# Performance work log

Measured on AMD Instinct MI355X. Metric: run time of the kernel, lower is better.

## Reference

```python
import jax, jax.numpy as jnp
import numpy as np

TOKEN_DIM = 512
ATTN_DIM = 512
NUM_HEADS = 8
MLP_SIZE = 2048
EPS = 1e-6


def setup_inputs() -> dict:
    key = jax.random.key(0)
    ks = jax.random.split(key, 9)
    s_tok = 1.0 / np.sqrt(TOKEN_DIM)
    s_att = 1.0 / np.sqrt(ATTN_DIM)
    s_mlp = 1.0 / np.sqrt(MLP_SIZE)
    return {
        "inputs": jax.random.normal(ks[0], (2, 4096, TOKEN_DIM), dtype=jnp.float32),
        "Wq": jax.random.uniform(ks[1], (TOKEN_DIM, ATTN_DIM), jnp.float32, -s_tok, s_tok),
        "Wk": jax.random.uniform(ks[2], (TOKEN_DIM, ATTN_DIM), jnp.float32, -s_tok, s_tok),
        "Wv": jax.random.uniform(ks[3], (TOKEN_DIM, ATTN_DIM), jnp.float32, -s_tok, s_tok),
        "Wo": jax.random.uniform(ks[4], (ATTN_DIM, TOKEN_DIM), jnp.float32, -s_att, s_att),
        "W1": jax.random.uniform(ks[5], (TOKEN_DIM, MLP_SIZE), jnp.float32, -s_tok, s_tok),
        "b1": jax.random.uniform(ks[6], (MLP_SIZE,), jnp.float32, -s_tok, s_tok),
        "W2": jax.random.uniform(ks[7], (MLP_SIZE, TOKEN_DIM), jnp.float32, -s_mlp, s_mlp),
        "b2": jax.random.uniform(ks[8], (TOKEN_DIM,), jnp.float32, -s_mlp, s_mlp),
        "ln_att_g": jnp.ones((TOKEN_DIM,), jnp.float32),
        "ln_att_b": jnp.zeros((TOKEN_DIM,), jnp.float32),
        "ln_mlp_g": jnp.ones((TOKEN_DIM,), jnp.float32),
        "ln_mlp_b": jnp.zeros((TOKEN_DIM,), jnp.float32),
    }


def _layernorm(x, g, b):
    mu = jnp.mean(x, axis=-1, keepdims=True)
    var = jnp.mean(jnp.square(x - mu), axis=-1, keepdims=True)
    return (x - mu) * jax.lax.rsqrt(var + EPS) * g + b


def _attention(x, Wq, Wk, Wv, Wo):
    B, N, _ = x.shape
    H, Dh = NUM_HEADS, ATTN_DIM // NUM_HEADS
    # project then split heads: (B, N, H, Dh) -> (B, H, N, Dh)
    q = (x @ Wq).reshape(B, N, H, Dh).transpose(0, 2, 1, 3)
    k = (x @ Wk).reshape(B, N, H, Dh).transpose(0, 2, 1, 3)
    v = (x @ Wv).reshape(B, N, H, Dh).transpose(0, 2, 1, 3)
    scale = Dh ** -0.5
    scores = jnp.einsum("bhnd,bhmd->bhnm", q, k) * scale  # full NxN scores
    attn = jax.nn.softmax(scores, axis=-1)
    out = jnp.einsum("bhnm,bhmd->bhnd", attn, v)
    out = out.transpose(0, 2, 1, 3).reshape(B, N, ATTN_DIM)
    return out @ Wo


def reference(inputs, Wq, Wk, Wv, Wo, W1, b1, W2, b2,
              ln_att_g, ln_att_b, ln_mlp_g, ln_mlp_b):
    x = _layernorm(inputs, ln_att_g, ln_att_b)
    x = _attention(x, Wq, Wk, Wv, Wo)
    y = x + inputs
    z = _layernorm(y, ln_mlp_g, ln_mlp_b)
    z = jax.nn.gelu(z @ W1 + b1, approximate=False) @ W2 + b2
    return z + y
```

## Files before the change

kernel.cpp:

```cpp
#include <hip/hip_runtime.h>
#include <hip/hip_bf16.h>
#include <cmath>


typedef unsigned short u16;
typedef float  f32x4  __attribute__((ext_vector_type(4)));
typedef short  bf16x8 __attribute__((ext_vector_type(8)));
typedef u16    u16x4  __attribute__((ext_vector_type(4)));

#define DEV __device__ __forceinline__
#define AS1(p) ((const __attribute__((address_space(1))) void*)(p))
#define AS3(p) ((__attribute__((address_space(3))) void*)(p))

static constexpr int Mrows = 8192;
static constexpr int Dtok  = 512;
static constexpr int Fmlp  = 2048;
static constexpr float LOG2E = 1.44269504088896340736f;

DEV u16 f2b(float f) {
  union { float f; unsigned u; } v; v.f = f;
  unsigned r = v.u + 0x7fffu + ((v.u >> 16) & 1u);
  return (u16)(r >> 16);
}

DEV unsigned cvtpk(float a, float b) {
  unsigned r;
  asm("v_cvt_pk_bf16_f32 %0, %1, %2" : "=v"(r) : "v"(a), "v"(b));
  return r;
}

DEV void plswap16(unsigned &a, unsigned &b) {
  asm("v_permlane16_swap_b32 %0, %1" : "+v"(a), "+v"(b));
}

DEV float ex2(float x) {
#if __has_builtin(__builtin_amdgcn_exp2f)
  return __builtin_amdgcn_exp2f(x);
#else
  float r; asm("v_exp_f32 %0, %1" : "=v"(r) : "v"(x)); return r;
#endif
}

DEV f32x4 mfma32(bf16x8 a, bf16x8 b, f32x4 c) {
  return __builtin_amdgcn_mfma_f32_16x16x32_bf16(a, b, c, 0, 0, 0);
}

__global__ __launch_bounds__(256) void convert_all(
    const float* __restrict__ Wq, const float* __restrict__ Wk,
    const float* __restrict__ Wv, const float* __restrict__ Wo,
    const float* __restrict__ W1, const float* __restrict__ W2,
    u16* __restrict__ Wqt, u16* __restrict__ Wkt, u16* __restrict__ Wvt,
    u16* __restrict__ Wot, u16* __restrict__ W1t, u16* __restrict__ W2t,
    float qscale) {
  int bid = blockIdx.x;
  const float* src; u16* dst; int K, N; float sc = 1.0f;
  if (bid < 1024)      { src = Wq; dst = Wqt; K = 512;  N = 512;  sc = qscale; }
  else if (bid < 2048) { src = Wk; dst = Wkt; K = 512;  N = 512;  bid -= 1024; }
  else if (bid < 3072) { src = Wv; dst = Wvt; K = 512;  N = 512;  bid -= 2048; }
  else if (bid < 4096) { src = Wo; dst = Wot; K = 512;  N = 512;  bid -= 3072; }
  else if (bid < 8192) { src = W1; dst = W1t; K = 512;  N = 2048; bid -= 4096; }
  else                 { src = W2; dst = W2t; K = 2048; N = 512;  bid -= 8192; }
  const int idx = bid * 256 + threadIdx.x;
  const int k = idx / N, n = idx - k * N;
  dst[(size_t)n * K + k] = f2b(src[idx] * sc);
}

__global__ __launch_bounds__(256) void ln_kernel(const float* __restrict__ x,
                                                 const float* __restrict__ g,
                                                 const float* __restrict__ b,
                                                 u16* __restrict__ o) {
  const int row = blockIdx.x, tid = threadIdx.x;
  float2 v = ((const float2*)(x + (size_t)row * 512))[tid];
  float s = v.x + v.y, ss = v.x * v.x + v.y * v.y;
#pragma unroll
  for (int off = 32; off > 0; off >>= 1) {
    s  += __shfl_down(s, off);
    ss += __shfl_down(ss, off);
  }
  __shared__ float ps[4], pss[4];
  const int wave = tid >> 6, lane = tid & 63;
  if (lane == 0) { ps[wave] = s; pss[wave] = ss; }
  __syncthreads();
  const float S  = ps[0] + ps[1] + ps[2] + ps[3];
  const float SS = pss[0] + pss[1] + pss[2] + pss[3];
  const float mean = S * (1.0f / 512.0f);
  const float var  = SS * (1.0f / 512.0f) - mean * mean;
  const float rstd = rsqrtf(var + 1e-6f);
  const float2 gg = ((const float2*)g)[tid];
  const float2 bb = ((const float2*)b)[tid];
  ushort2 ov;
  ov.x = f2b((v.x - mean) * rstd * gg.x + bb.x);
  ov.y = f2b((v.y - mean) * rstd * gg.y + bb.y);
  ((ushort2*)(o + (size_t)row * 512))[tid] = ov;
}

template <int EPI, int BM>
__global__ __launch_bounds__(256) void gemm_kernel(
    const u16* __restrict__ A, const u16* __restrict__ Bt,
    u16* __restrict__ outb, u16* __restrict__ outbK, u16* __restrict__ outbV,
    float* __restrict__ outf,
    const float* __restrict__ bias, const float* __restrict__ resid,
    int M, int N, int K) {
  __shared__ u16 Al[BM * 32];
  __shared__ u16 Bl[128 * 32];
  constexpr int WM = BM / 2;
  const int tid = threadIdx.x;
  const int wave = tid >> 6, lane = tid & 63;
  const int lhi = lane >> 4, llo = lane & 15;
  const int wr = wave >> 1, wc = wave & 1;
  const int m0 = blockIdx.y * BM, n0 = blockIdx.x * 128;

  f32x4 acc[BM / 32][4] = {};

  for (int k0 = 0; k0 < K; k0 += 32) {
#pragma unroll
    for (int i = 0; i < BM / 64; ++i) {
      const int rb = i * 64 + wave * 16;
      const u16* sa = A + (size_t)(m0 + rb + (lane >> 2)) * K + k0 + (lane & 3) * 8;
      __builtin_amdgcn_global_load_lds(AS1(sa), AS3(&Al[rb * 32]), 16, 0, 0);
    }
#pragma unroll
    for (int i = 0; i < 2; ++i) {
      const int rb = i * 64 + wave * 16;
      const u16* sb = Bt + (size_t)(n0 + rb + (lane >> 2)) * K + k0 + (lane & 3) * 8;
      __builtin_amdgcn_global_load_lds(AS1(sb), AS3(&Bl[rb * 32]), 16, 0, 0);
    }
    __syncthreads();
    bf16x8 af[BM / 32], bfr[4];
#pragma unroll
    for (int mi = 0; mi < BM / 32; ++mi)
      af[mi] = *(const bf16x8*)&Al[(wr * WM + mi * 16 + llo) * 32 + lhi * 8];
#pragma unroll
    for (int ni = 0; ni < 4; ++ni)
      bfr[ni] = *(const bf16x8*)&Bl[(wc * 64 + ni * 16 + llo) * 32 + lhi * 8];
#pragma unroll
    for (int mi = 0; mi < BM / 32; ++mi)
#pragma unroll
      for (int ni = 0; ni < 4; ++ni)
        acc[mi][ni] = __builtin_amdgcn_mfma_f32_16x16x32_bf16(af[mi], bfr[ni],
                                                              acc[mi][ni], 0, 0, 0);
    __syncthreads();
  }

  if constexpr (EPI == 5) {
    if (n0 < 1024) {
      u16* dst = (n0 < 512) ? outb : outbK;
      const int c0 = (n0 & 511) + wc * 64;
#pragma unroll
      for (int mi = 0; mi < BM / 32; ++mi)
#pragma unroll
        for (int r = 0; r < 4; ++r) {
          const size_t grow = (size_t)m0 + wr * WM + mi * 16 + lhi * 4 + r;
#pragma unroll
          for (int ni = 0; ni < 4; ++ni)
            dst[grow * 512 + c0 + ni * 16 + llo] = f2b(acc[mi][ni][r]);
        }
    } else {
      const int bb = m0 >> 12;
      const int nb = (m0 & 4095) + wr * WM + lhi * 4;
#pragma unroll
      for (int mi = 0; mi < BM / 32; ++mi)
#pragma unroll
        for (int ni = 0; ni < 4; ++ni) {
          const int gcol = (n0 - 1024) + wc * 64 + ni * 16 + llo;
          u16x4 pk;
#pragma unroll
          for (int r = 0; r < 4; ++r) pk[r] = f2b(acc[mi][ni][r]);
          u16* dst = outbV + (((size_t)(bb * 8 + (gcol >> 6))) * 64 + (gcol & 63)) * 4096
                           + nb + mi * 16;
          *(u16x4*)dst = pk;
        }
    }
  } else {
#pragma unroll
    for (int mi = 0; mi < BM / 32; ++mi) {
#pragma unroll
      for (int r = 0; r < 4; ++r) {
        const size_t grow = (size_t)m0 + wr * WM + mi * 16 + lhi * 4 + r;
#pragma unroll
        for (int ni = 0; ni < 4; ++ni) {
          const int gcol = n0 + wc * 64 + ni * 16 + llo;
          float v = acc[mi][ni][r];
          if (EPI == 0) {
            outb[grow * N + gcol] = f2b(v);
          } else if (EPI == 1) {
            v += bias[gcol];
            v = 0.5f * v * (1.0f + erff(v * 0.70710678118654752f));
            outb[grow * N + gcol] = f2b(v);
          } else if (EPI == 2) {
            v += resid[grow * N + gcol];
            outf[grow * N + gcol] = v;
          } else {
            v += bias[gcol] + resid[grow * N + gcol];
            outf[grow * N + gcol] = v;
          }
        }
      }
    }
  }
}

__global__ __launch_bounds__(256) void attn_kernel(const u16* __restrict__ Q,
                                                   const u16* __restrict__ Kg,
                                                   const u16* __restrict__ VT,
                                                   u16* __restrict__ O) {
  const int qt = blockIdx.x, bh = blockIdx.y;
  const int b = bh >> 3, h = bh & 7;
  const int tid = threadIdx.x, wave = tid >> 6, lane = tid & 63;
  const int lhi = lane >> 4, llo = lane & 15;

  __shared__ u16 Kl[2][4096];
  __shared__ u16 Vl[2][4096];

  const size_t rowbase = (size_t)b * 4096;
  const int col0 = h * 64;
  const int q0 = qt * 128;

  bf16x8 qf0[2], qf1[2];
  {
    const u16* qp0 = Q + (rowbase + q0 + wave * 32 + llo) * 512 + col0 + lhi * 8;
    qf0[0] = *(const bf16x8*)qp0;
    qf0[1] = *(const bf16x8*)(qp0 + 32);
    const u16* qp1 = qp0 + (size_t)16 * 512;
    qf1[0] = *(const bf16x8*)qp1;
    qf1[1] = *(const bf16x8*)(qp1 + 32);
  }

  const int srow8 = lane >> 3;
  const int kcsw  = ((lane & 7) ^ srow8) * 8;
  const u16* kbase0 = Kg + (rowbase + wave * 16 + srow8) * 512 + col0 + kcsw;
  const u16* kbase1 = kbase0 + (size_t)8 * 512;
  const u16* vbase0 = VT + ((size_t)bh * 64 + wave * 16 + srow8) * 4096 + kcsw;
  const u16* vbase1 = vbase0 + (size_t)8 * 4096;

  const int xr = (llo & 7) << 4;
  const int ka0 = (16 * lhi) ^ xr;
  const int ka1 = (16 * (4 + lhi)) ^ xr;
  const int csig = ((lhi & 1) << 1) | (lhi >> 1);
  const int vb0 = 16 * (csig ^ (llo & 7));
  const int vb1 = 16 * ((csig | 4) ^ (llo & 7));

  const bf16x8 ones = {(short)0x3F80, (short)0x3F80, (short)0x3F80, (short)0x3F80,
                       (short)0x3F80, (short)0x3F80, (short)0x3F80, (short)0x3F80};

  f32x4 o0[4] = {}, o1[4] = {};
  f32x4 o40 = {}, o41 = {};

  auto stage = [&](int kvr, int B) {
    __builtin_amdgcn_global_load_lds(AS1(kbase0 + (size_t)kvr * 512),
                                     AS3(&Kl[B][wave * 1024]), 16, 0, 0);
    __builtin_amdgcn_global_load_lds(AS1(kbase1 + (size_t)kvr * 512),
                                     AS3(&Kl[B][wave * 1024 + 512]), 16, 0, 0);
    __builtin_amdgcn_global_load_lds(AS1(vbase0 + kvr),
                                     AS3(&Vl[B][wave * 1024]), 16, 0, 0);
    __builtin_amdgcn_global_load_lds(AS1(vbase1 + kvr),
                                     AS3(&Vl[B][wave * 1024 + 512]), 16, 0, 0);
  };

  auto packP = [&](const f32x4* stj, bf16x8& Bv0, bf16x8& Bv1) {
    unsigned a0 = cvtpk(ex2(stj[0][0]), ex2(stj[0][1]));
    unsigned a1 = cvtpk(ex2(stj[0][2]), ex2(stj[0][3]));
    unsigned b0 = cvtpk(ex2(stj[1][0]), ex2(stj[1][1]));
    unsigned b1 = cvtpk(ex2(stj[1][2]), ex2(stj[1][3]));
    unsigned c0 = cvtpk(ex2(stj[2][0]), ex2(stj[2][1]));
    unsigned c1 = cvtpk(ex2(stj[2][2]), ex2(stj[2][3]));
    unsigned d0 = cvtpk(ex2(stj[3][0]), ex2(stj[3][1]));
    unsigned d1 = cvtpk(ex2(stj[3][2]), ex2(stj[3][3]));
    plswap16(a0, b0); plswap16(a1, b1);
    plswap16(c0, d0); plswap16(c1, d1);
    union UB { unsigned u[4]; bf16x8 v; } X, Y;
    X.u[0] = a0; X.u[1] = a1; X.u[2] = b0; X.u[3] = b1;
    Y.u[0] = c0; Y.u[1] = c1; Y.u[2] = d0; Y.u[3] = d1;
    Bv0 = X.v; Bv1 = Y.v;
  };

  auto compute = [&](int B) {
    const char* klb = (const char*)&Kl[B][0] + llo * 128;
    const char* vlb = (const char*)&Vl[B][0] + llo * 128;
    f32x4 st0[4], st1[4];
    __builtin_amdgcn_s_setprio(1);
#pragma unroll
    for (int jt = 0; jt < 4; ++jt) {
      bf16x8 kf0 = *(const bf16x8*)(klb + jt * 2048 + ka0);
      bf16x8 kf1 = *(const bf16x8*)(klb + jt * 2048 + ka1);
      f32x4 z0 = {}, z1 = {};
      z0 = mfma32(kf0, qf0[0], z0); z0 = mfma32(kf1, qf0[1], z0);
      z1 = mfma32(kf0, qf1[0], z1); z1 = mfma32(kf1, qf1[1], z1);
      st0[jt] = z0; st1[jt] = z1;
    }
    __builtin_amdgcn_s_setprio(0);
    bf16x8 P00, P01, P10, P11;
    packP(st0, P00, P01);
    packP(st1, P10, P11);
    __builtin_amdgcn_s_setprio(1);
    o40 = mfma32(ones, P00, o40); o40 = mfma32(ones, P01, o40);
    o41 = mfma32(ones, P10, o41); o41 = mfma32(ones, P11, o41);
#pragma unroll
    for (int dt = 0; dt < 4; ++dt) {
      bf16x8 vf0 = *(const bf16x8*)(vlb + dt * 2048 + vb0);
      bf16x8 vf1 = *(const bf16x8*)(vlb + dt * 2048 + vb1);
      o0[dt] = mfma32(vf0, P00, o0[dt]); o0[dt] = mfma32(vf1, P01, o0[dt]);
      o1[dt] = mfma32(vf0, P10, o1[dt]); o1[dt] = mfma32(vf1, P11, o1[dt]);
    }
    __builtin_amdgcn_s_setprio(0);
  };

  stage(0, 0);
  __syncthreads();
  for (int kv0 = 0; kv0 < 4096; kv0 += 128) {
    stage(kv0 + 64, 1);
    compute(0);
    __syncthreads();
    if (kv0 + 128 < 4096) stage(kv0 + 128, 0);
    compute(1);
    __syncthreads();
  }

  {
    const float inv = 1.0f / o40[0];
    u16* op = O + (rowbase + q0 + wave * 32 + llo) * 512 + col0 + 4 * lhi;
#pragma unroll
    for (int dt = 0; dt < 4; ++dt) {
      u16x4 pk;
#pragma unroll
      for (int r = 0; r < 4; ++r) pk[r] = f2b(o0[dt][r] * inv);
      *(u16x4*)(op + dt * 16) = pk;
    }
  }
  {
    const float inv = 1.0f / o41[0];
    u16* op = O + (rowbase + q0 + wave * 32 + 16 + llo) * 512 + col0 + 4 * lhi;
#pragma unroll
    for (int dt = 0; dt < 4; ++dt) {
      u16x4 pk;
#pragma unroll
      for (int r = 0; r < 4; ++r) pk[r] = f2b(o1[dt][r] * inv);
      *(u16x4*)(op + dt * 16) = pk;
    }
  }
}

extern "C" void kernel_launch(void* const* d_in, const int* in_sizes, int n_in,
                              void* d_out, int out_size, void* d_ws, size_t ws_size,
                              hipStream_t stream) {
  const float* inputs = (const float*)d_in[0];
  const float* Wq  = (const float*)d_in[1];
  const float* Wk  = (const float*)d_in[2];
  const float* Wv  = (const float*)d_in[3];
  const float* Wo  = (const float*)d_in[4];
  const float* W1  = (const float*)d_in[5];
  const float* b1  = (const float*)d_in[6];
  const float* W2  = (const float*)d_in[7];
  const float* b2  = (const float*)d_in[8];
  const float* g1  = (const float*)d_in[9];
  const float* be1 = (const float*)d_in[10];
  const float* g2  = (const float*)d_in[11];
  const float* be2 = (const float*)d_in[12];
  float* out = (float*)d_out;

  const int M = Mrows, D = Dtok, F = Fmlp;

  char* w = (char*)d_ws;
  u16* xln  = (u16*)w;  w += (size_t)M * D * 2;
  u16* Qb   = (u16*)w;  w += (size_t)M * D * 2;
  u16* Kb   = (u16*)w;  w += (size_t)M * D * 2;
  u16* VT   = (u16*)w;  w += (size_t)M * D * 2;
  u16* attn = (u16*)w;  w += (size_t)M * D * 2;
  float* y  = (float*)w; w += (size_t)M * D * 4;
  u16* Wqt  = (u16*)w;  w += (size_t)D * D * 2;
  u16* Wkt  = (u16*)w;  w += (size_t)D * D * 2;
  u16* Wvt  = (u16*)w;  w += (size_t)D * D * 2;
  u16* Wot  = (u16*)w;  w += (size_t)D * D * 2;
  u16* W1t  = (u16*)w;  w += (size_t)D * F * 2;
  u16* W2t  = (u16*)w;  w += (size_t)F * D * 2;
  u16* zln = xln;
  u16* h1  = Qb;

  convert_all<<<dim3(12288), 256, 0, stream>>>(Wq, Wk, Wv, Wo, W1, W2,
                                               Wqt, Wkt, Wvt, Wot, W1t, W2t,
                                               0.125f * LOG2E);

  ln_kernel<<<dim3(M), 256, 0, stream>>>(inputs, g1, be1, xln);

  gemm_kernel<5, 128><<<dim3(12, M / 128), 256, 0, stream>>>(
      xln, Wqt, Qb, Kb, VT, nullptr, nullptr, nullptr, M, 512, D);

  attn_kernel<<<dim3(32, 16), 256, 0, stream>>>(Qb, Kb, VT, attn);

  gemm_kernel<2, 64><<<dim3(4, M / 64), 256, 0, stream>>>(
      attn, Wot, nullptr, nullptr, nullptr, y, nullptr, inputs, M, D, D);

  ln_kernel<<<dim3(M), 256, 0, stream>>>(y, g2, be2, zln);

  gemm_kernel<1, 128><<<dim3(16, M / 128), 256, 0, stream>>>(
      zln, W1t, h1, nullptr, nullptr, nullptr, b1, nullptr, M, F, D);
  gemm_kernel<3, 64><<<dim3(4, M / 64), 256, 0, stream>>>(
      h1, W2t, nullptr, nullptr, nullptr, out, b2, y, M, D, F);
}
```

Before: 243.3 us.

## Double-buffer GEMM LDS, fuse LN1 into convert, bf16 residual, fast GELU

The GEMM main loop now uses two LDS buffers so the next K-slice is staged while MFMAs run on the current one, with one barrier per slice instead of two. The first layernorm is folded into the weight-conversion launch, removing one kernel launch. The post-attention residual y is stored as bf16 instead of fp32, which halves its write and its two reads, and the second layernorm reads bf16. The erf-based GELU is replaced by an exp2/rcp sigmoid-style approximation. Storing y in bf16 and approximating GELU both reduce precision.

```diff
diff --git a/kernel.cpp b/kernel.cpp
--- a/kernel.cpp
+++ b/kernel.cpp
@@ -21,6 +21,10 @@
   union { float f; unsigned u; } v; v.f = f;
   unsigned r = v.u + 0x7fffu + ((v.u >> 16) & 1u);
   return (u16)(r >> 16);
+}
+
+DEV float b2f(u16 x) {
+  union { unsigned u; float f; } v; v.u = ((unsigned)x) << 16; return v.f;
 }
 
 DEV unsigned cvtpk(float a, float b) {
@@ -41,18 +45,59 @@
 #endif
 }
 
+DEV float rcp(float x) {
+  float r; asm("v_rcp_f32 %0, %1" : "=v"(r) : "v"(x)); return r;
+}
+
+DEV float gelu(float x) {
+  const float u = x * x;
+  float z = x * (2.30225828f + 0.10295048f * u);
+  z = fminf(z, 80.0f);
+  const float E = ex2(z);
+  return x * E * rcp(E + 1.0f);
+}
+
 DEV f32x4 mfma32(bf16x8 a, bf16x8 b, f32x4 c) {
   return __builtin_amdgcn_mfma_f32_16x16x32_bf16(a, b, c, 0, 0, 0);
 }
 
-__global__ __launch_bounds__(256) void convert_all(
+__global__ __launch_bounds__(256) void convert_ln(
     const float* __restrict__ Wq, const float* __restrict__ Wk,
     const float* __restrict__ Wv, const float* __restrict__ Wo,
     const float* __restrict__ W1, const float* __restrict__ W2,
     u16* __restrict__ Wqt, u16* __restrict__ Wkt, u16* __restrict__ Wvt,
     u16* __restrict__ Wot, u16* __restrict__ W1t, u16* __restrict__ W2t,
-    float qscale) {
+    float qscale,
+    const float* __restrict__ xin, const float* __restrict__ g1,
+    const float* __restrict__ be1, u16* __restrict__ xln) {
   int bid = blockIdx.x;
+  const int tid = threadIdx.x;
+  if (bid >= 12288) {
+    const int row = bid - 12288;
+    float2 v = ((const float2*)(xin + (size_t)row * 512))[tid];
+    float s = v.x + v.y, ss = v.x * v.x + v.y * v.y;
+#pragma unroll
+    for (int off = 32; off > 0; off >>= 1) {
+      s  += __shfl_down(s, off);
+      ss += __shfl_down(ss, off);
+    }
+    __shared__ float ps[4], pss[4];
+    const int wave = tid >> 6, lane = tid & 63;
+    if (lane == 0) { ps[wave] = s; pss[wave] = ss; }
+    __syncthreads();
+    const float S  = ps[0] + ps[1] + ps[2] + ps[3];
+    const float SS = pss[0] + pss[1] + pss[2] + pss[3];
+    const float mean = S * (1.0f / 512.0f);
+    const float var  = SS * (1.0f / 512.0f) - mean * mean;
+    const float rstd = rsqrtf(var + 1e-6f);
+    const float2 gg = ((const float2*)g1)[tid];
+    const float2 bb = ((const float2*)be1)[tid];
+    ushort2 ov;
+    ov.x = f2b((v.x - mean) * rstd * gg.x + bb.x);
+    ov.y = f2b((v.y - mean) * rstd * gg.y + bb.y);
+    ((ushort2*)(xln + (size_t)row * 512))[tid] = ov;
+    return;
+  }
   const float* src; u16* dst; int K, N; float sc = 1.0f;
   if (bid < 1024)      { src = Wq; dst = Wqt; K = 512;  N = 512;  sc = qscale; }
   else if (bid < 2048) { src = Wk; dst = Wkt; K = 512;  N = 512;  bid -= 1024; }
@@ -60,18 +105,19 @@
   else if (bid < 4096) { src = Wo; dst = Wot; K = 512;  N = 512;  bid -= 3072; }
   else if (bid < 8192) { src = W1; dst = W1t; K = 512;  N = 2048; bid -= 4096; }
   else                 { src = W2; dst = W2t; K = 2048; N = 512;  bid -= 8192; }
-  const int idx = bid * 256 + threadIdx.x;
+  const int idx = bid * 256 + tid;
   const int k = idx / N, n = idx - k * N;
   dst[(size_t)n * K + k] = f2b(src[idx] * sc);
 }
 
-__global__ __launch_bounds__(256) void ln_kernel(const float* __restrict__ x,
-                                                 const float* __restrict__ g,
-                                                 const float* __restrict__ b,
-                                                 u16* __restrict__ o) {
+__global__ __launch_bounds__(256) void ln_bf16(const u16* __restrict__ x,
+                                               const float* __restrict__ g,
+                                               const float* __restrict__ b,
+                                               u16* __restrict__ o) {
   const int row = blockIdx.x, tid = threadIdx.x;
-  float2 v = ((const float2*)(x + (size_t)row * 512))[tid];
-  float s = v.x + v.y, ss = v.x * v.x + v.y * v.y;
+  const ushort2 v2 = ((const ushort2*)(x + (size_t)row * 512))[tid];
+  const float vx = b2f(v2.x), vy = b2f(v2.y);
+  float s = vx + vy, ss = vx * vx + vy * vy;
 #pragma unroll
   for (int off = 32; off > 0; off >>= 1) {
     s  += __shfl_down(s, off);
@@ -89,8 +135,8 @@
   const float2 gg = ((const float2*)g)[tid];
   const float2 bb = ((const float2*)b)[tid];
   ushort2 ov;
-  ov.x = f2b((v.x - mean) * rstd * gg.x + bb.x);
-  ov.y = f2b((v.y - mean) * rstd * gg.y + bb.y);
+  ov.x = f2b((vx - mean) * rstd * gg.x + bb.x);
+  ov.y = f2b((vy - mean) * rstd * gg.y + bb.y);
   ((ushort2*)(o + (size_t)row * 512))[tid] = ov;
 }
 
@@ -99,10 +145,11 @@
     const u16* __restrict__ A, const u16* __restrict__ Bt,
     u16* __restrict__ outb, u16* __restrict__ outbK, u16* __restrict__ outbV,
     float* __restrict__ outf,
-    const float* __restrict__ bias, const float* __restrict__ resid,
+    const float* __restrict__ bias,
+    const float* __restrict__ residf, const u16* __restrict__ residb,
     int M, int N, int K) {
-  __shared__ u16 Al[BM * 32];
-  __shared__ u16 Bl[128 * 32];
+  __shared__ u16 Al[2][BM * 32];
+  __shared__ u16 Bl[2][128 * 32];
   constexpr int WM = BM / 2;
   const int tid = threadIdx.x;
   const int wave = tid >> 6, lane = tid & 63;
@@ -112,33 +159,45 @@
 
   f32x4 acc[BM / 32][4] = {};
 
-  for (int k0 = 0; k0 < K; k0 += 32) {
+  auto stageG = [&](int k0, int Bf) {
 #pragma unroll
     for (int i = 0; i < BM / 64; ++i) {
       const int rb = i * 64 + wave * 16;
       const u16* sa = A + (size_t)(m0 + rb + (lane >> 2)) * K + k0 + (lane & 3) * 8;
-      __builtin_amdgcn_global_load_lds(AS1(sa), AS3(&Al[rb * 32]), 16, 0, 0);
+      __builtin_amdgcn_global_load_lds(AS1(sa), AS3(&Al[Bf][rb * 32]), 16, 0, 0);
     }
 #pragma unroll
     for (int i = 0; i < 2; ++i) {
       const int rb = i * 64 + wave * 16;
       const u16* sb = Bt + (size_t)(n0 + rb + (lane >> 2)) * K + k0 + (lane & 3) * 8;
-      __builtin_amdgcn_global_load_lds(AS1(sb), AS3(&Bl[rb * 32]), 16, 0, 0);
-    }
-    __syncthreads();
+      __builtin_amdgcn_global_load_lds(AS1(sb), AS3(&Bl[Bf][rb * 32]), 16, 0, 0);
+    }
+  };
+
+  auto computeG = [&](int Bf) {
     bf16x8 af[BM / 32], bfr[4];
 #pragma unroll
     for (int mi = 0; mi < BM / 32; ++mi)
-      af[mi] = *(const bf16x8*)&Al[(wr * WM + mi * 16 + llo) * 32 + lhi * 8];
+      af[mi] = *(const bf16x8*)&Al[Bf][(wr * WM + mi * 16 + llo) * 32 + lhi * 8];
 #pragma unroll
     for (int ni = 0; ni < 4; ++ni)
-      bfr[ni] = *(const bf16x8*)&Bl[(wc * 64 + ni * 16 + llo) * 32 + lhi * 8];
+      bfr[ni] = *(const bf16x8*)&Bl[Bf][(wc * 64 + ni * 16 + llo) * 32 + lhi * 8];
 #pragma unroll
     for (int mi = 0; mi < BM / 32; ++mi)
 #pragma unroll
       for (int ni = 0; ni < 4; ++ni)
         acc[mi][ni] = __builtin_amdgcn_mfma_f32_16x16x32_bf16(af[mi], bfr[ni],
                                                               acc[mi][ni], 0, 0, 0);
+  };
+
+  stageG(0, 0);
+  __syncthreads();
+  for (int k0 = 0; k0 < K; k0 += 64) {
+    stageG(k0 + 32, 1);
+    computeG(0);
+    __syncthreads();
+    if (k0 + 64 < K) stageG(k0 + 64, 0);
+    computeG(1);
     __syncthreads();
   }
 
@@ -181,17 +240,14 @@
         for (int ni = 0; ni < 4; ++ni) {
           const int gcol = n0 + wc * 64 + ni * 16 + llo;
           float v = acc[mi][ni][r];
-          if (EPI == 0) {
-            outb[grow * N + gcol] = f2b(v);
-          } else if (EPI == 1) {
-            v += bias[gcol];
-            v = 0.5f * v * (1.0f + erff(v * 0.70710678118654752f));
+          if (EPI == 1) {
+            v = gelu(v + bias[gcol]);
             outb[grow * N + gcol] = f2b(v);
           } else if (EPI == 2) {
-            v += resid[grow * N + gcol];
-            outf[grow * N + gcol] = v;
+            v += residf[grow * N + gcol];
+            outb[grow * N + gcol] = f2b(v);
           } else {
-            v += bias[gcol] + resid[grow * N + gcol];
+            v += bias[gcol] + b2f(residb[grow * N + gcol]);
             outf[grow * N + gcol] = v;
           }
         }
@@ -366,7 +422,7 @@
   u16* Kb   = (u16*)w;  w += (size_t)M * D * 2;
   u16* VT   = (u16*)w;  w += (size_t)M * D * 2;
   u16* attn = (u16*)w;  w += (size_t)M * D * 2;
-  float* y  = (float*)w; w += (size_t)M * D * 4;
+  u16* yb   = (u16*)w;  w += (size_t)M * D * 2;
   u16* Wqt  = (u16*)w;  w += (size_t)D * D * 2;
   u16* Wkt  = (u16*)w;  w += (size_t)D * D * 2;
   u16* Wvt  = (u16*)w;  w += (size_t)D * D * 2;
@@ -376,24 +432,22 @@
   u16* zln = xln;
   u16* h1  = Qb;
 
-  convert_all<<<dim3(12288), 256, 0, stream>>>(Wq, Wk, Wv, Wo, W1, W2,
-                                               Wqt, Wkt, Wvt, Wot, W1t, W2t,
-                                               0.125f * LOG2E);
-
-  ln_kernel<<<dim3(M), 256, 0, stream>>>(inputs, g1, be1, xln);
+  convert_ln<<<dim3(12288 + 8192), 256, 0, stream>>>(
+      Wq, Wk, Wv, Wo, W1, W2, Wqt, Wkt, Wvt, Wot, W1t, W2t,
+      0.125f * LOG2E, inputs, g1, be1, xln);
 
   gemm_kernel<5, 128><<<dim3(12, M / 128), 256, 0, stream>>>(
-      xln, Wqt, Qb, Kb, VT, nullptr, nullptr, nullptr, M, 512, D);
+      xln, Wqt, Qb, Kb, VT, nullptr, nullptr, nullptr, nullptr, M, 512, D);
 
   attn_kernel<<<dim3(32, 16), 256, 0, stream>>>(Qb, Kb, VT, attn);
 
   gemm_kernel<2, 64><<<dim3(4, M / 64), 256, 0, stream>>>(
-      attn, Wot, nullptr, nullptr, nullptr, y, nullptr, inputs, M, D, D);
-
-  ln_kernel<<<dim3(M), 256, 0, stream>>>(y, g2, be2, zln);
+      attn, Wot, yb, nullptr, nullptr, nullptr, nullptr, inputs, nullptr, M, D, D);
+
+  ln_bf16<<<dim3(M), 256, 0, stream>>>(yb, g2, be2, zln);
 
   gemm_kernel<1, 128><<<dim3(16, M / 128), 256, 0, stream>>>(
-      zln, W1t, h1, nullptr, nullptr, nullptr, b1, nullptr, M, F, D);
+      zln, W1t, h1, nullptr, nullptr, nullptr, b1, nullptr, nullptr, M, F, D);
   gemm_kernel<3, 64><<<dim3(4, M / 64), 256, 0, stream>>>(
-      h1, W2t, nullptr, nullptr, nullptr, out, b2, y, M, D, F);
-}
+      h1, W2t, nullptr, nullptr, nullptr, out, b2, nullptr, yb, M, D, F);
+}
```

Measured after the change: 227.9 us. 6.3% less time.
